# Kernel tuning notes

Hardware: AMD Instinct MI355X
Metric: run time of the kernel (lower is better)

## Reference

```python
import jax, jax.numpy as jnp
import numpy as np

STRIDE = 1
PADDING = 1
GROUPS = 1


def setup_inputs() -> dict:
    key = jax.random.key(0)
    kx, kw, kb = jax.random.split(key, 3)
    x_int = jax.random.randint(kx, (16, 256, 56, 56), 0, 127, dtype=jnp.int32)
    weight_int = jax.random.randint(kw, (256, 256, 3, 3), 0, 127, dtype=jnp.int32)
    bias_int = jax.random.randint(kb, (256,), 0, 127, dtype=jnp.int32)
    return {"x_int": x_int, "weight_int": weight_int, "bias_int": bias_int}


def reference(x_int, weight_int, bias_int):
    # Integer conv2d with int32 accumulation, exactly F.conv2d semantics.
    y = jax.lax.conv_general_dilated(
        x_int,
        weight_int,
        window_strides=(STRIDE, STRIDE),
        padding=((PADDING, PADDING), (PADDING, PADDING)),
        dimension_numbers=("NCHW", "OIHW", "NCHW"),
        feature_group_count=GROUPS,
    )
    # bias broadcast over [B, Cout, H, W]
    return y + bias_int[None, :, None, None]
```

## Files before the change

kernel.cpp:

```cpp
#include <hip/hip_runtime.h>


typedef int v4i __attribute__((ext_vector_type(4)));

#define X8_ROWSTRIDE 4640
#define X8_IMGSTRIDE 269120
#define X8_BYTES (64 * X8_IMGSTRIDE)
#define W8_TILE 36864
#define WLS_BYTES 36864
#define XS_OFF WLS_BYTES
#define LDS_BYTES 65536

typedef const __attribute__((address_space(1))) unsigned char* gptr_t;
typedef __attribute__((address_space(3))) unsigned char* lptr_t;

__global__ __launch_bounds__(256)
void pack_x(const int* __restrict__ x, unsigned char* __restrict__ x8) {
  const int ih = blockIdx.x;
  const int b  = blockIdx.y;
  for (int gid = threadIdx.x; gid < 896; gid += 256) {
    const int slot  = gid % 56;
    const int cg    = gid / 56;
    const int chunk = cg >> 2;
    const int gr    = cg & 3;
    const int* xp = x + ((b * 256 + chunk * 64 + gr * 16) * 56 + ih) * 56 + slot;
    union { v4i v; unsigned char c[16]; } u;
    #pragma unroll
    for (int j = 0; j < 16; ++j) u.c[j] = (unsigned char)xp[j * 3136];
    *(v4i*)(x8 + (chunk * 16 + b) * X8_IMGSTRIDE + (ih + 1) * X8_ROWSTRIDE
          + (slot + 1) * 80 + gr * 16) = u.v;
  }
}

__global__ __launch_bounds__(256)
void zero_halo(unsigned char* __restrict__ x8) {
  unsigned char* base = x8 + blockIdx.x * X8_IMGSTRIDE;
  for (int e = threadIdx.x; e < 1140; e += 256) {
    int off;
    if (e < 580) {
      const int half = e < 290 ? 0 : 1;
      const int g = e - half * 290;
      off = half * (57 * X8_ROWSTRIDE) + g * 16;
    } else {
      const int f = e - 580;
      const int r = f / 10 + 1;
      const int pos = f - (r - 1) * 10;
      const int side = pos / 5, g = pos - side * 5;
      off = r * X8_ROWSTRIDE + side * (57 * 80) + g * 16;
    }
    *(v4i*)(base + off) = (v4i){0, 0, 0, 0};
  }
}

__global__ __launch_bounds__(256)
void pack_w(const int* __restrict__ wgt, unsigned char* __restrict__ w8) {
  const int id = blockIdx.x * 256 + threadIdx.x;
  const int co = id / 2304;
  const int r  = id - co * 2304;
  const int ci = r / 9;
  const int s  = r - ci * 9;
  const int tc = co >> 6, co64 = co & 63, chunk = ci >> 6, ci64 = ci & 63;
  w8[(((tc * 4 + chunk) * 64 + co64) * 576) + s * 64 + ci64] = (unsigned char)wgt[id];
}

__global__ __launch_bounds__(512, 4)
void conv_main(const unsigned char* __restrict__ ws8, const int* __restrict__ bias,
               int* __restrict__ out) {
  __shared__ __align__(16) unsigned char lds[LDS_BYTES];
  unsigned char* wls = lds;
  unsigned char* xs  = lds + XS_OFF;
  const unsigned char* x8 = ws8;
  const unsigned char* w8 = ws8 + X8_BYTES;

  const int tid = threadIdx.x, lane = tid & 63, wv = tid >> 6;
  const int q = lane >> 4, m = lane & 15;
  const int cw = wv & 1;
  const int pw = wv >> 1;
  const int tc = blockIdx.x;
  const int h0 = blockIdx.y * 4;
  const int b  = blockIdx.z;

  v4i acc[2][4];
  #pragma unroll
  for (int i = 0; i < 2; ++i)
    #pragma unroll
    for (int j = 0; j < 4; ++j) acc[i][j] = (v4i){0, 0, 0, 0};

  for (int c = 0; c < 4; ++c) {
    __syncthreads();
    const unsigned char* wg = w8 + (tc * 4 + c) * W8_TILE;
    #pragma unroll
    for (int i = 0; i < 5; ++i) {
      const int j = i * 8 + wv;
      if (j < 36)
        __builtin_amdgcn_global_load_lds((gptr_t)(wg + j * 1024 + lane * 16),
                                         (lptr_t)(wls + j * 1024), 16, 0, 0);
    }
    const unsigned char* xg = x8 + (c * 16 + b) * X8_IMGSTRIDE + h0 * X8_ROWSTRIDE;
    #pragma unroll
    for (int i = 0; i < 4; ++i) {
      const int j = i * 8 + wv;
      if (j < 28)
        __builtin_amdgcn_global_load_lds((gptr_t)(xg + j * 1024 + lane * 16),
                                         (lptr_t)(xs + j * 1024), 16, 0, 0);
    }
    __syncthreads();
    const unsigned char* arow = wls + (cw * 32 + m) * 576 + q * 16;
    #pragma unroll
    for (int kh = 0; kh < 3; ++kh) {
      const unsigned char* xr = xs + (pw + kh) * X8_ROWSTRIDE + q * 16;
      #pragma unroll
      for (int kw = 0; kw < 3; ++kw) {
        const int s = kh * 3 + kw;
        const v4i a0 = *(const v4i*)(arow + s * 64);
        const v4i a1 = *(const v4i*)(arow + 16 * 576 + s * 64);
        #pragma unroll
        for (int nt = 0; nt < 4; ++nt) {
          int idx = nt * 16 + m + kw;
          idx = idx > 57 ? 57 : idx;
          const v4i bf = *(const v4i*)(xr + idx * 80);
          acc[0][nt] = __builtin_amdgcn_mfma_i32_16x16x64_i8(a0, bf, acc[0][nt], 0, 0, 0);
          acc[1][nt] = __builtin_amdgcn_mfma_i32_16x16x64_i8(a1, bf, acc[1][nt], 0, 0, 0);
        }
      }
    }
  }

  const int h = h0 + pw;
  #pragma unroll
  for (int half = 0; half < 2; ++half) {
    #pragma unroll
    for (int nt = 0; nt < 4; ++nt) {
      const int wp = nt * 16 + m;
      if (wp < 56) {
        #pragma unroll
        for (int r = 0; r < 4; ++r) {
          const int co = tc * 64 + cw * 32 + half * 16 + q * 4 + r;
          out[((b * 256 + co) * 56 + h) * 56 + wp] = acc[half][nt][r] + bias[co];
        }
      }
    }
  }
}

extern "C" void kernel_launch(void* const* d_in, const int* in_sizes, int n_in,
                              void* d_out, int out_size, void* d_ws, size_t ws_size,
                              hipStream_t stream) {
  const int* x    = (const int*)d_in[0];
  const int* w    = (const int*)d_in[1];
  const int* bias = (const int*)d_in[2];
  unsigned char* ws8 = (unsigned char*)d_ws;
  hipLaunchKernelGGL(pack_x,    dim3(56, 16), dim3(256), 0, stream, x, ws8);
  hipLaunchKernelGGL(zero_halo, dim3(64),     dim3(256), 0, stream, ws8);
  hipLaunchKernelGGL(pack_w,    dim3(2304),   dim3(256), 0, stream, w, ws8 + X8_BYTES);
  hipLaunchKernelGGL(conv_main, dim3(4, 14, 16), dim3(512), 0, stream,
                     ws8, bias, (int*)d_out);
}
```

Measured before the change: 146.7 us.

## Swizzle packed int8 activation/weight layout and fuse packing kernels into one launch

Repacks the int8 activations with a 64-byte slot stride instead of an 80-byte padded stride. The 16-byte channel group inside each slot is rotated by slot index, and the weight rows get the same rotation, so LDS reads for the MFMA B operand stay free of bank conflicts without padding. This shrinks each staged input row and cuts the global-to-LDS copy per chunk from 28 KB to 22 KB. The activation pack, halo zeroing and weight pack are merged into one kernel that writes zero borders inline, removing two launches. LDS B-fragment offsets are precomputed into registers, which may add register pressure.

```diff
diff --git a/kernel.cpp b/kernel.cpp
--- a/kernel.cpp
+++ b/kernel.cpp
@@ -3,64 +3,54 @@
 
 typedef int v4i __attribute__((ext_vector_type(4)));
 
-#define X8_ROWSTRIDE 4640
-#define X8_IMGSTRIDE 269120
+#define X8_ROWSTRIDE 3712
+#define X8_IMGSTRIDE (58 * X8_ROWSTRIDE)
 #define X8_BYTES (64 * X8_IMGSTRIDE)
 #define W8_TILE 36864
-#define WLS_BYTES 36864
-#define XS_OFF WLS_BYTES
-#define LDS_BYTES 65536
+#define XS_OFF 36864
+#define LDS_BYTES 59648
 
 typedef const __attribute__((address_space(1))) unsigned char* gptr_t;
 typedef __attribute__((address_space(3))) unsigned char* lptr_t;
 
 __global__ __launch_bounds__(256)
-void pack_x(const int* __restrict__ x, unsigned char* __restrict__ x8) {
-  const int ih = blockIdx.x;
-  const int b  = blockIdx.y;
-  for (int gid = threadIdx.x; gid < 896; gid += 256) {
-    const int slot  = gid % 56;
-    const int cg    = gid / 56;
-    const int chunk = cg >> 2;
-    const int gr    = cg & 3;
-    const int* xp = x + ((b * 256 + chunk * 64 + gr * 16) * 56 + ih) * 56 + slot;
+void pack_all(const int* __restrict__ x, const int* __restrict__ wgt,
+              unsigned char* __restrict__ ws8) {
+  const int blk = blockIdx.x;
+  if (blk < 3712) {
+    const int row = blk % 58;
+    const int cb  = blk / 58;
+    const int chunk = cb >> 4, b = cb & 15;
+    const int tid = threadIdx.x;
+    if (tid >= 232) return;
+    const int slot = tid >> 2, p = tid & 3;
+    union { v4i v; unsigned char c[16]; } u;
+    u.v = (v4i){0, 0, 0, 0};
+    if (row >= 1 && row <= 56 && slot >= 1 && slot <= 56) {
+      const int q = (p - (slot >> 2)) & 3;
+      const unsigned char* src = (const unsigned char*)(x
+          + ((b * 256 + chunk * 64 + q * 16) * 56 + (row - 1)) * 56 + (slot - 1));
+      #pragma unroll
+      for (int j = 0; j < 16; ++j) u.c[j] = src[j * 12544];
+    }
+    *(v4i*)(ws8 + cb * X8_IMGSTRIDE + row * X8_ROWSTRIDE + slot * 64 + p * 16) = u.v;
+  } else {
+    const int g  = (blk - 3712) * 256 + threadIdx.x;
+    const int p  = g & 3;
+    const int sp = g >> 2;
+    const int s  = sp % 9;
+    const int ct = sp / 9;
+    const int co64 = ct & 63;
+    const int tcch = ct >> 6;
+    const int tc = tcch >> 2, chunk = tcch & 3;
+    const int q = (p - ((co64 >> 2) & 3)) & 3;
+    const unsigned char* src = (const unsigned char*)(wgt
+        + (tc * 64 + co64) * 2304 + (chunk * 64 + q * 16) * 9 + s);
     union { v4i v; unsigned char c[16]; } u;
     #pragma unroll
-    for (int j = 0; j < 16; ++j) u.c[j] = (unsigned char)xp[j * 3136];
-    *(v4i*)(x8 + (chunk * 16 + b) * X8_IMGSTRIDE + (ih + 1) * X8_ROWSTRIDE
-          + (slot + 1) * 80 + gr * 16) = u.v;
+    for (int j = 0; j < 16; ++j) u.c[j] = src[j * 36];
+    *(v4i*)(ws8 + X8_BYTES + ct * 576 + s * 64 + p * 16) = u.v;
   }
-}
-
-__global__ __launch_bounds__(256)
-void zero_halo(unsigned char* __restrict__ x8) {
-  unsigned char* base = x8 + blockIdx.x * X8_IMGSTRIDE;
-  for (int e = threadIdx.x; e < 1140; e += 256) {
-    int off;
-    if (e < 580) {
-      const int half = e < 290 ? 0 : 1;
-      const int g = e - half * 290;
-      off = half * (57 * X8_ROWSTRIDE) + g * 16;
-    } else {
-      const int f = e - 580;
-      const int r = f / 10 + 1;
-      const int pos = f - (r - 1) * 10;
-      const int side = pos / 5, g = pos - side * 5;
-      off = r * X8_ROWSTRIDE + side * (57 * 80) + g * 16;
-    }
-    *(v4i*)(base + off) = (v4i){0, 0, 0, 0};
-  }
-}
-
-__global__ __launch_bounds__(256)
-void pack_w(const int* __restrict__ wgt, unsigned char* __restrict__ w8) {
-  const int id = blockIdx.x * 256 + threadIdx.x;
-  const int co = id / 2304;
-  const int r  = id - co * 2304;
-  const int ci = r / 9;
-  const int s  = r - ci * 9;
-  const int tc = co >> 6, co64 = co & 63, chunk = ci >> 6, ci64 = ci & 63;
-  w8[(((tc * 4 + chunk) * 64 + co64) * 576) + s * 64 + ci64] = (unsigned char)wgt[id];
 }
 
 __global__ __launch_bounds__(512, 4)
@@ -80,6 +70,17 @@
   const int h0 = blockIdx.y * 4;
   const int b  = blockIdx.z;
 
+  const unsigned char* arow = wls + (cw * 32 + m) * 576 + ((q + (m >> 2)) & 3) * 16;
+  int boff[3][4];
+  #pragma unroll
+  for (int kw = 0; kw < 3; ++kw)
+    #pragma unroll
+    for (int nt = 0; nt < 4; ++nt) {
+      int slot = nt * 16 + m + kw;
+      slot = slot > 57 ? 57 : slot;
+      boff[kw][nt] = slot * 64 + ((q + (slot >> 2)) & 3) * 16;
+    }
+
   v4i acc[2][4];
   #pragma unroll
   for (int i = 0; i < 2; ++i)
@@ -98,17 +99,16 @@
     }
     const unsigned char* xg = x8 + (c * 16 + b) * X8_IMGSTRIDE + h0 * X8_ROWSTRIDE;
     #pragma unroll
-    for (int i = 0; i < 4; ++i) {
+    for (int i = 0; i < 3; ++i) {
       const int j = i * 8 + wv;
-      if (j < 28)
+      if (j < 22)
         __builtin_amdgcn_global_load_lds((gptr_t)(xg + j * 1024 + lane * 16),
                                          (lptr_t)(xs + j * 1024), 16, 0, 0);
     }
     __syncthreads();
-    const unsigned char* arow = wls + (cw * 32 + m) * 576 + q * 16;
     #pragma unroll
     for (int kh = 0; kh < 3; ++kh) {
-      const unsigned char* xr = xs + (pw + kh) * X8_ROWSTRIDE + q * 16;
+      const unsigned char* xr = xs + (pw + kh) * X8_ROWSTRIDE;
       #pragma unroll
       for (int kw = 0; kw < 3; ++kw) {
         const int s = kh * 3 + kw;
@@ -116,9 +116,7 @@
         const v4i a1 = *(const v4i*)(arow + 16 * 576 + s * 64);
         #pragma unroll
         for (int nt = 0; nt < 4; ++nt) {
-          int idx = nt * 16 + m + kw;
-          idx = idx > 57 ? 57 : idx;
-          const v4i bf = *(const v4i*)(xr + idx * 80);
+          const v4i bf = *(const v4i*)(xr + boff[kw][nt]);
           acc[0][nt] = __builtin_amdgcn_mfma_i32_16x16x64_i8(a0, bf, acc[0][nt], 0, 0, 0);
           acc[1][nt] = __builtin_amdgcn_mfma_i32_16x16x64_i8(a1, bf, acc[1][nt], 0, 0, 0);
         }
@@ -150,9 +148,7 @@
   const int* w    = (const int*)d_in[1];
   const int* bias = (const int*)d_in[2];
   unsigned char* ws8 = (unsigned char*)d_ws;
-  hipLaunchKernelGGL(pack_x,    dim3(56, 16), dim3(256), 0, stream, x, ws8);
-  hipLaunchKernelGGL(zero_halo, dim3(64),     dim3(256), 0, stream, ws8);
-  hipLaunchKernelGGL(pack_w,    dim3(2304),   dim3(256), 0, stream, w, ws8 + X8_BYTES);
+  hipLaunchKernelGGL(pack_all, dim3(3712 + 144), dim3(256), 0, stream, x, w, ws8);
   hipLaunchKernelGGL(conv_main, dim3(4, 14, 16), dim3(512), 0, stream,
                      ws8, bias, (int*)d_out);
 }
```

After: 136.2 us. 7.1% less time.
